# Optimization experiments

Measured on AMD Instinct MI355X. Metric: run time of the kernel, lower is better.

The kernel has to match this reference:

```python
import jax, jax.numpy as jnp
import numpy as np

N_NODES = 10000
IN_FEAT = 512
OUT_FEAT = 512
N_EDGES = 160000


def setup_inputs() -> dict:
    key = jax.random.key(0)
    kx, kw, ks, kd = jax.random.split(key, 4)
    x = jax.random.normal(kx, (N_NODES, IN_FEAT), dtype=jnp.float32)
    # Xavier-uniform init for w: shape [out_features, 2*in_features]
    fan_in, fan_out = 2 * IN_FEAT, OUT_FEAT
    limit = float(np.sqrt(6.0 / (fan_in + fan_out)))
    w = jax.random.uniform(kw, (OUT_FEAT, 2 * IN_FEAT), dtype=jnp.float32,
                           minval=-limit, maxval=limit)
    src = jax.random.randint(ks, (N_EDGES,), 0, N_NODES, dtype=jnp.int32)
    dst = jax.random.randint(kd, (N_EDGES,), 0, N_NODES, dtype=jnp.int32)
    edge_index = jnp.stack([src, dst], axis=0)  # [2, E]
    return {"x": x, "w": w, "edge_index": edge_index}


def reference(x, w, edge_index):
    # GraphSAGE-mean layer: h = relu(W @ concat(x, mean_{j in N(i)} x_j))
    src, dst = edge_index[0], edge_index[1]
    msgs = x[src]  # [E, F] gather of neighbor features
    summed = jax.ops.segment_sum(msgs, dst, num_segments=x.shape[0])  # [N, F]
    deg = jax.ops.segment_sum(jnp.ones_like(dst, dtype=x.dtype), dst,
                              num_segments=x.shape[0])  # [N]
    neighbor_mean = summed / jnp.maximum(deg, 1.0)[:, None]
    message = jnp.concatenate([x, neighbor_mean], axis=-1)  # [N, 2F]
    weighted = jnp.einsum('of,nf->no', w, message)  # [N, out]
    return jax.nn.relu(weighted)
```

## Files before the change

kernel.cpp:

```cpp
#include <hip/hip_runtime.h>
#include <hip/hip_bf16.h>

#define N_NODES 10000
#define IN_FEAT 512
#define OUT_FEAT 512
#define N_EDGES 160000
#define KDIM 1024
#define CAP 96

typedef __bf16 bf16x8 __attribute__((ext_vector_type(8)));
typedef float f32x4 __attribute__((ext_vector_type(4)));

#define AS1 __attribute__((address_space(1)))
#define AS3 __attribute__((address_space(3)))

__device__ __forceinline__ void async_copy16(void* lds, const void* g) {
    __builtin_amdgcn_global_load_lds((const AS1 unsigned int*)g,
                                     (AS3 unsigned int*)lds, 16, 0, 0);
}

__device__ __forceinline__ unsigned short f2bf(float f) {
    unsigned int u = __builtin_bit_cast(unsigned int, f);
    u += 0x7fffu + ((u >> 16) & 1u);
    return (unsigned short)(u >> 16);
}


__global__ __launch_bounds__(256) void k_zero(int* __restrict__ cnt) {
    int i = blockIdx.x * 256 + threadIdx.x;
    if (i < N_NODES / 4) ((int4*)cnt)[i] = (int4){0, 0, 0, 0};
}


#define PREP_EDGE_BLOCKS ((N_EDGES + 255) / 256)
#define PREP_W_BLOCKS (OUT_FEAT * KDIM / 8 / 256)
#define PREP_X_BLOCKS (N_NODES * IN_FEAT / 8 / 256)
#define PREP_BLOCKS (PREP_EDGE_BLOCKS + PREP_W_BLOCKS + PREP_X_BLOCKS)

__device__ __forceinline__ void cvt8(const float* __restrict__ src,
                                     unsigned short* __restrict__ dst, int i) {
    const float4* sp = (const float4*)(src + (size_t)i * 8);
    float4 a = sp[0], b = sp[1];
    uint4 o;
    o.x = (unsigned)f2bf(a.x) | ((unsigned)f2bf(a.y) << 16);
    o.y = (unsigned)f2bf(a.z) | ((unsigned)f2bf(a.w) << 16);
    o.z = (unsigned)f2bf(b.x) | ((unsigned)f2bf(b.y) << 16);
    o.w = (unsigned)f2bf(b.z) | ((unsigned)f2bf(b.w) << 16);
    *(uint4*)(dst + (size_t)i * 8) = o;
}

__global__ __launch_bounds__(256) void k_prep(
    const float* __restrict__ x, const float* __restrict__ w,
    const int* __restrict__ ei, int* __restrict__ cnt,
    int* __restrict__ bucket, unsigned short* __restrict__ xb,
    unsigned short* __restrict__ wb) {
    int b = blockIdx.x;
    if (b < PREP_EDGE_BLOCKS) {
        int e = b * 256 + threadIdx.x;
        if (e < N_EDGES) {
            int s = ei[e];
            int d = ei[N_EDGES + e];
            int slot = atomicAdd(&cnt[d], 1);
            if (slot < CAP) bucket[d * CAP + slot] = s;
        }
    } else if (b < PREP_EDGE_BLOCKS + PREP_W_BLOCKS) {
        int i = (b - PREP_EDGE_BLOCKS) * 256 + threadIdx.x;
        cvt8(w, wb, i);
    } else {
        int i = (b - PREP_EDGE_BLOCKS - PREP_W_BLOCKS) * 256 + threadIdx.x;
        cvt8(x, xb, i);
    }
}


__device__ __forceinline__ void accum8(float* acc, uint4 v) {
    unsigned d[4] = {v.x, v.y, v.z, v.w};
#pragma unroll
    for (int j = 0; j < 4; ++j) {
        acc[2 * j]     += __builtin_bit_cast(float, d[j] << 16);
        acc[2 * j + 1] += __builtin_bit_cast(float, d[j] & 0xffff0000u);
    }
}

__global__ __launch_bounds__(256) void k_aggregate(
    const unsigned short* __restrict__ xb, const int* __restrict__ cnt,
    const int* __restrict__ bucket, unsigned short* __restrict__ mb) {
    int wid = (blockIdx.x * 256 + threadIdx.x) >> 6;
    int lane = threadIdx.x & 63;
    if (wid >= N_NODES) return;
    int deg = cnt[wid];
    int n = deg < CAP ? deg : CAP;
    const int4* brow = (const int4*)(bucket + wid * CAP);
    const unsigned short* xrow = xb + lane * 8;
    float acc[8] = {0.f, 0.f, 0.f, 0.f, 0.f, 0.f, 0.f, 0.f};
    int e = 0;
    for (; e + 8 <= n; e += 8) {
        int4 i0 = brow[e >> 2];
        int4 i1 = brow[(e >> 2) + 1];
        uint4 v0 = *(const uint4*)(xrow + (size_t)i0.x * IN_FEAT);
        uint4 v1 = *(const uint4*)(xrow + (size_t)i0.y * IN_FEAT);
        uint4 v2 = *(const uint4*)(xrow + (size_t)i0.z * IN_FEAT);
        uint4 v3 = *(const uint4*)(xrow + (size_t)i0.w * IN_FEAT);
        uint4 v4 = *(const uint4*)(xrow + (size_t)i1.x * IN_FEAT);
        uint4 v5 = *(const uint4*)(xrow + (size_t)i1.y * IN_FEAT);
        uint4 v6 = *(const uint4*)(xrow + (size_t)i1.z * IN_FEAT);
        uint4 v7 = *(const uint4*)(xrow + (size_t)i1.w * IN_FEAT);
        accum8(acc, v0); accum8(acc, v1); accum8(acc, v2); accum8(acc, v3);
        accum8(acc, v4); accum8(acc, v5); accum8(acc, v6); accum8(acc, v7);
    }
    if (e + 4 <= n) {
        int4 i0 = brow[e >> 2];
        uint4 v0 = *(const uint4*)(xrow + (size_t)i0.x * IN_FEAT);
        uint4 v1 = *(const uint4*)(xrow + (size_t)i0.y * IN_FEAT);
        uint4 v2 = *(const uint4*)(xrow + (size_t)i0.z * IN_FEAT);
        uint4 v3 = *(const uint4*)(xrow + (size_t)i0.w * IN_FEAT);
        accum8(acc, v0); accum8(acc, v1); accum8(acc, v2); accum8(acc, v3);
        e += 4;
    }
    for (; e < n; ++e) {
        int s = bucket[wid * CAP + e];
        uint4 v = *(const uint4*)(xrow + (size_t)s * IN_FEAT);
        accum8(acc, v);
    }
    float inv = 1.0f / fmaxf((float)deg, 1.0f);
    uint4 o;
    o.x = (unsigned)f2bf(acc[0] * inv) | ((unsigned)f2bf(acc[1] * inv) << 16);
    o.y = (unsigned)f2bf(acc[2] * inv) | ((unsigned)f2bf(acc[3] * inv) << 16);
    o.z = (unsigned)f2bf(acc[4] * inv) | ((unsigned)f2bf(acc[5] * inv) << 16);
    o.w = (unsigned)f2bf(acc[6] * inv) | ((unsigned)f2bf(acc[7] * inv) << 16);
    *(uint4*)(mb + (size_t)wid * IN_FEAT + lane * 8) = o;
}


#define BM 64
#define BN 128
#define BK 64

__global__ __launch_bounds__(256) void k_gemm(const unsigned short* __restrict__ xb,
                                              const unsigned short* __restrict__ mb,
                                              const unsigned short* __restrict__ wb,
                                              float* __restrict__ out) {
    __shared__ unsigned short As[BM * BK];
    __shared__ unsigned short Bs[BN * BK];
    const int tid = threadIdx.x;
    const int lane = tid & 63;
    const int w = tid >> 6;
    const int m0 = blockIdx.x * BM;
    const int n0 = blockIdx.y * BN;

    const int wr = w >> 1, wc = w & 1;

    const int st_sub = lane >> 3;
    const int st_col = (lane & 7) * 8;

    f32x4 acc[2][4];
#pragma unroll
    for (int m = 0; m < 2; ++m)
#pragma unroll
        for (int n = 0; n < 4; ++n) acc[m][n] = (f32x4){0.f, 0.f, 0.f, 0.f};

    for (int k0 = 0; k0 < KDIM; k0 += BK) {
        const unsigned short* abase = (k0 < IN_FEAT) ? xb : mb;
        const int kc = (k0 < IN_FEAT) ? k0 : (k0 - IN_FEAT);
#pragma unroll
        for (int i = 0; i < 2; ++i) {
            int row = w * 16 + i * 8 + st_sub;
            int rg = m0 + row;
            if (rg > N_NODES - 1) rg = N_NODES - 1;
            async_copy16(&As[(w * 16 + i * 8) * BK],
                         abase + (size_t)rg * IN_FEAT + kc + st_col);
        }
#pragma unroll
        for (int i = 0; i < 4; ++i) {
            int row = w * 32 + i * 8 + st_sub;
            async_copy16(&Bs[(w * 32 + i * 8) * BK],
                         wb + (size_t)(n0 + row) * KDIM + k0 + st_col);
        }
        __syncthreads();

#pragma unroll
        for (int kk = 0; kk < 2; ++kk) {
            bf16x8 a[2], b[4];
            const int krow = kk * 32 + (lane >> 4) * 8;
#pragma unroll
            for (int m = 0; m < 2; ++m) {
                int r = wr * 32 + m * 16 + (lane & 15);
                a[m] = *(const bf16x8*)&As[r * BK + krow];
            }
#pragma unroll
            for (int n = 0; n < 4; ++n) {
                int r = wc * 64 + n * 16 + (lane & 15);
                b[n] = *(const bf16x8*)&Bs[r * BK + krow];
            }
#pragma unroll
            for (int m = 0; m < 2; ++m)
#pragma unroll
                for (int n = 0; n < 4; ++n)
                    acc[m][n] = __builtin_amdgcn_mfma_f32_16x16x32_bf16(
                        a[m], b[n], acc[m][n], 0, 0, 0);
        }
        __syncthreads();
    }

    const int col_in = lane & 15;
    const int rquad = (lane >> 4) * 4;
#pragma unroll
    for (int m = 0; m < 2; ++m) {
#pragma unroll
        for (int n = 0; n < 4; ++n) {
#pragma unroll
            for (int r = 0; r < 4; ++r) {
                int mg = m0 + wr * 32 + m * 16 + rquad + r;
                int og = n0 + wc * 64 + n * 16 + col_in;
                if (mg < N_NODES) {
                    float v = acc[m][n][r];
                    out[(size_t)mg * OUT_FEAT + og] = v > 0.f ? v : 0.f;
                }
            }
        }
    }
}


extern "C" void kernel_launch(void* const* d_in, const int* in_sizes, int n_in,
                              void* d_out, int out_size, void* d_ws, size_t ws_size,
                              hipStream_t stream) {
    const float* x = (const float*)d_in[0];
    const float* w = (const float*)d_in[1];
    const int* ei = (const int*)d_in[2];
    float* out = (float*)d_out;

    char* ws = (char*)d_ws;
    const size_t XB_OFF = 0;
    const size_t MB_OFF = XB_OFF + (size_t)N_NODES * IN_FEAT * 2;
    const size_t WB_OFF = MB_OFF + (size_t)N_NODES * IN_FEAT * 2;
    const size_t CNT_OFF = WB_OFF + (size_t)OUT_FEAT * KDIM * 2;
    const size_t BKT_OFF = CNT_OFF + (size_t)N_NODES * 4;

    unsigned short* xb = (unsigned short*)(ws + XB_OFF);
    unsigned short* mb = (unsigned short*)(ws + MB_OFF);
    unsigned short* wb = (unsigned short*)(ws + WB_OFF);
    int* cnt = (int*)(ws + CNT_OFF);
    int* bucket = (int*)(ws + BKT_OFF);

    k_zero<<<(N_NODES / 4 + 255) / 256, 256, 0, stream>>>(cnt);
    k_prep<<<PREP_BLOCKS, 256, 0, stream>>>(x, w, ei, cnt, bucket, xb, wb);
    k_aggregate<<<(N_NODES * 64 + 255) / 256, 256, 0, stream>>>(xb, cnt, bucket, mb);
    dim3 ggrid((N_NODES + BM - 1) / BM, OUT_FEAT / BN);
    k_gemm<<<ggrid, 256, 0, stream>>>(xb, mb, wb, out);
}
```

Measured before the change: 71.93 us.

## Split aggregation across feature chunks and swizzle GEMM tile order for locality

The aggregation kernel now spreads each node over four blocks along a second grid dimension. Each lane loads one 32-bit word (two bf16 values) per neighbor instead of a 16-byte vector, which raises the number of waves in flight and cuts per-thread register pressure. The GEMM launch becomes a 1D grid with a swizzled mapping that groups 8 M-tiles with all 4 N-tiles, so neighboring blocks share A and B tiles in cache; blocks past the last M-tile exit early. In exchange, each gather load is narrower, so more load instructions and more bucket index reads are issued per byte of neighbor data.

```diff
diff --git a/kernel.cpp b/kernel.cpp
--- a/kernel.cpp
+++ b/kernel.cpp
@@ -23,6 +23,13 @@
     unsigned int u = __builtin_bit_cast(unsigned int, f);
     u += 0x7fffu + ((u >> 16) & 1u);
     return (unsigned short)(u >> 16);
+}
+
+__device__ __forceinline__ float bflo(unsigned v) {
+    return __builtin_bit_cast(float, v << 16);
+}
+__device__ __forceinline__ float bfhi(unsigned v) {
+    return __builtin_bit_cast(float, v & 0xffff0000u);
 }
 
 
@@ -73,68 +80,59 @@
 }
 
 
-__device__ __forceinline__ void accum8(float* acc, uint4 v) {
-    unsigned d[4] = {v.x, v.y, v.z, v.w};
-#pragma unroll
-    for (int j = 0; j < 4; ++j) {
-        acc[2 * j]     += __builtin_bit_cast(float, d[j] << 16);
-        acc[2 * j + 1] += __builtin_bit_cast(float, d[j] & 0xffff0000u);
-    }
-}
-
 __global__ __launch_bounds__(256) void k_aggregate(
     const unsigned short* __restrict__ xb, const int* __restrict__ cnt,
     const int* __restrict__ bucket, unsigned short* __restrict__ mb) {
-    int wid = (blockIdx.x * 256 + threadIdx.x) >> 6;
-    int lane = threadIdx.x & 63;
-    if (wid >= N_NODES) return;
-    int deg = cnt[wid];
-    int n = deg < CAP ? deg : CAP;
-    const int4* brow = (const int4*)(bucket + wid * CAP);
-    const unsigned short* xrow = xb + lane * 8;
-    float acc[8] = {0.f, 0.f, 0.f, 0.f, 0.f, 0.f, 0.f, 0.f};
+    const int chunk = blockIdx.y;
+    const int node = blockIdx.x * 4 + (threadIdx.x >> 6);
+    const int lane = threadIdx.x & 63;
+    const int deg = cnt[node];
+    const int n = deg < CAP ? deg : CAP;
+    const int4* brow = (const int4*)(bucket + node * CAP);
+    const unsigned* xcol = (const unsigned*)xb + chunk * 64 + lane;
+    float a0 = 0.f, a1 = 0.f;
     int e = 0;
     for (; e + 8 <= n; e += 8) {
         int4 i0 = brow[e >> 2];
         int4 i1 = brow[(e >> 2) + 1];
-        uint4 v0 = *(const uint4*)(xrow + (size_t)i0.x * IN_FEAT);
-        uint4 v1 = *(const uint4*)(xrow + (size_t)i0.y * IN_FEAT);
-        uint4 v2 = *(const uint4*)(xrow + (size_t)i0.z * IN_FEAT);
-        uint4 v3 = *(const uint4*)(xrow + (size_t)i0.w * IN_FEAT);
-        uint4 v4 = *(const uint4*)(xrow + (size_t)i1.x * IN_FEAT);
-        uint4 v5 = *(const uint4*)(xrow + (size_t)i1.y * IN_FEAT);
-        uint4 v6 = *(const uint4*)(xrow + (size_t)i1.z * IN_FEAT);
-        uint4 v7 = *(const uint4*)(xrow + (size_t)i1.w * IN_FEAT);
-        accum8(acc, v0); accum8(acc, v1); accum8(acc, v2); accum8(acc, v3);
-        accum8(acc, v4); accum8(acc, v5); accum8(acc, v6); accum8(acc, v7);
+        unsigned v0 = xcol[(size_t)i0.x * 256];
+        unsigned v1 = xcol[(size_t)i0.y * 256];
+        unsigned v2 = xcol[(size_t)i0.z * 256];
+        unsigned v3 = xcol[(size_t)i0.w * 256];
+        unsigned v4 = xcol[(size_t)i1.x * 256];
+        unsigned v5 = xcol[(size_t)i1.y * 256];
+        unsigned v6 = xcol[(size_t)i1.z * 256];
+        unsigned v7 = xcol[(size_t)i1.w * 256];
+        a0 += bflo(v0) + bflo(v1) + bflo(v2) + bflo(v3) +
+              bflo(v4) + bflo(v5) + bflo(v6) + bflo(v7);
+        a1 += bfhi(v0) + bfhi(v1) + bfhi(v2) + bfhi(v3) +
+              bfhi(v4) + bfhi(v5) + bfhi(v6) + bfhi(v7);
     }
     if (e + 4 <= n) {
         int4 i0 = brow[e >> 2];
-        uint4 v0 = *(const uint4*)(xrow + (size_t)i0.x * IN_FEAT);
-        uint4 v1 = *(const uint4*)(xrow + (size_t)i0.y * IN_FEAT);
-        uint4 v2 = *(const uint4*)(xrow + (size_t)i0.z * IN_FEAT);
-        uint4 v3 = *(const uint4*)(xrow + (size_t)i0.w * IN_FEAT);
-        accum8(acc, v0); accum8(acc, v1); accum8(acc, v2); accum8(acc, v3);
+        unsigned v0 = xcol[(size_t)i0.x * 256];
+        unsigned v1 = xcol[(size_t)i0.y * 256];
+        unsigned v2 = xcol[(size_t)i0.z * 256];
+        unsigned v3 = xcol[(size_t)i0.w * 256];
+        a0 += bflo(v0) + bflo(v1) + bflo(v2) + bflo(v3);
+        a1 += bfhi(v0) + bfhi(v1) + bfhi(v2) + bfhi(v3);
         e += 4;
     }
     for (; e < n; ++e) {
-        int s = bucket[wid * CAP + e];
-        uint4 v = *(const uint4*)(xrow + (size_t)s * IN_FEAT);
-        accum8(acc, v);
+        unsigned v = xcol[(size_t)bucket[node * CAP + e] * 256];
+        a0 += bflo(v);
+        a1 += bfhi(v);
     }
     float inv = 1.0f / fmaxf((float)deg, 1.0f);
-    uint4 o;
-    o.x = (unsigned)f2bf(acc[0] * inv) | ((unsigned)f2bf(acc[1] * inv) << 16);
-    o.y = (unsigned)f2bf(acc[2] * inv) | ((unsigned)f2bf(acc[3] * inv) << 16);
-    o.z = (unsigned)f2bf(acc[4] * inv) | ((unsigned)f2bf(acc[5] * inv) << 16);
-    o.w = (unsigned)f2bf(acc[6] * inv) | ((unsigned)f2bf(acc[7] * inv) << 16);
-    *(uint4*)(mb + (size_t)wid * IN_FEAT + lane * 8) = o;
+    unsigned o = (unsigned)f2bf(a0 * inv) | ((unsigned)f2bf(a1 * inv) << 16);
+    ((unsigned*)mb)[(size_t)node * 256 + chunk * 64 + lane] = o;
 }
 
 
 #define BM 64
 #define BN 128
 #define BK 64
+#define MT_PAD 160
 
 __global__ __launch_bounds__(256) void k_gemm(const unsigned short* __restrict__ xb,
                                               const unsigned short* __restrict__ mb,
@@ -142,12 +140,16 @@
                                               float* __restrict__ out) {
     __shared__ unsigned short As[BM * BK];
     __shared__ unsigned short Bs[BN * BK];
+    const int idx = blockIdx.x;
+    const int mt = (idx & 7) + 8 * (idx >> 5);
+    const int nt = (idx >> 3) & 3;
+    if (mt >= (N_NODES + BM - 1) / BM) return;
+    const int m0 = mt * BM;
+    const int n0 = nt * BN;
+
     const int tid = threadIdx.x;
     const int lane = tid & 63;
     const int w = tid >> 6;
-    const int m0 = blockIdx.x * BM;
-    const int n0 = blockIdx.y * BN;
-
     const int wr = w >> 1, wc = w & 1;
 
     const int st_sub = lane >> 3;
@@ -245,7 +247,7 @@
 
     k_zero<<<(N_NODES / 4 + 255) / 256, 256, 0, stream>>>(cnt);
     k_prep<<<PREP_BLOCKS, 256, 0, stream>>>(x, w, ei, cnt, bucket, xb, wb);
-    k_aggregate<<<(N_NODES * 64 + 255) / 256, 256, 0, stream>>>(xb, cnt, bucket, mb);
-    dim3 ggrid((N_NODES + BM - 1) / BM, OUT_FEAT / BN);
-    k_gemm<<<ggrid, 256, 0, stream>>>(xb, mb, wb, out);
-}
+    dim3 agrid(N_NODES / 4, 4);
+    k_aggregate<<<agrid, 256, 0, stream>>>(xb, cnt, bucket, mb);
+    k_gemm<<<(MT_PAD / 8) * 32, 256, 0, stream>>>(xb, mb, wb, out);
+}
```

New measurement: 73.40 us. 2.0% more time.

## Split neighbor aggregation across feature chunks and edge slots with shuffle reduction

Applied to the files above, without the earlier changes.

The aggregate kernel now gives each wavefront one node and one 128-feature chunk, with four lane groups each handling a different edge slot. Partial sums are combined with cross-lane xor shuffles before writing. This launches four times as many wavefronts with shorter dependent gather chains, aiming to raise memory-level parallelism and occupancy. The cost is extra shuffle work, repeated bucket index loads across chunks, and fewer loads in flight per lane.

```diff
diff --git a/kernel.cpp b/kernel.cpp
--- a/kernel.cpp
+++ b/kernel.cpp
@@ -85,50 +85,52 @@
 __global__ __launch_bounds__(256) void k_aggregate(
     const unsigned short* __restrict__ xb, const int* __restrict__ cnt,
     const int* __restrict__ bucket, unsigned short* __restrict__ mb) {
-    int wid = (blockIdx.x * 256 + threadIdx.x) >> 6;
-    int lane = threadIdx.x & 63;
-    if (wid >= N_NODES) return;
-    int deg = cnt[wid];
-    int n = deg < CAP ? deg : CAP;
-    const int4* brow = (const int4*)(bucket + wid * CAP);
-    const unsigned short* xrow = xb + lane * 8;
+    const int chunk = blockIdx.y;
+    const int node = blockIdx.x * 4 + (threadIdx.x >> 6);
+    const int lane = threadIdx.x & 63;
+    const int slot = lane >> 4;
+    const int fg = lane & 15;
+    const int deg = cnt[node];
+    const int n = deg < CAP ? deg : CAP;
+    const int bbase = node * CAP;
+    const unsigned short* xcol = xb + chunk * 128 + fg * 8;
     float acc[8] = {0.f, 0.f, 0.f, 0.f, 0.f, 0.f, 0.f, 0.f};
     int e = 0;
     for (; e + 8 <= n; e += 8) {
-        int4 i0 = brow[e >> 2];
-        int4 i1 = brow[(e >> 2) + 1];
-        uint4 v0 = *(const uint4*)(xrow + (size_t)i0.x * IN_FEAT);
-        uint4 v1 = *(const uint4*)(xrow + (size_t)i0.y * IN_FEAT);
-        uint4 v2 = *(const uint4*)(xrow + (size_t)i0.z * IN_FEAT);
-        uint4 v3 = *(const uint4*)(xrow + (size_t)i0.w * IN_FEAT);
-        uint4 v4 = *(const uint4*)(xrow + (size_t)i1.x * IN_FEAT);
-        uint4 v5 = *(const uint4*)(xrow + (size_t)i1.y * IN_FEAT);
-        uint4 v6 = *(const uint4*)(xrow + (size_t)i1.z * IN_FEAT);
-        uint4 v7 = *(const uint4*)(xrow + (size_t)i1.w * IN_FEAT);
-        accum8(acc, v0); accum8(acc, v1); accum8(acc, v2); accum8(acc, v3);
-        accum8(acc, v4); accum8(acc, v5); accum8(acc, v6); accum8(acc, v7);
+        int s0 = bucket[bbase + e + slot];
+        int s1 = bucket[bbase + e + 4 + slot];
+        uint4 v0 = *(const uint4*)(xcol + (size_t)s0 * IN_FEAT);
+        uint4 v1 = *(const uint4*)(xcol + (size_t)s1 * IN_FEAT);
+        accum8(acc, v0);
+        accum8(acc, v1);
     }
     if (e + 4 <= n) {
-        int4 i0 = brow[e >> 2];
-        uint4 v0 = *(const uint4*)(xrow + (size_t)i0.x * IN_FEAT);
-        uint4 v1 = *(const uint4*)(xrow + (size_t)i0.y * IN_FEAT);
-        uint4 v2 = *(const uint4*)(xrow + (size_t)i0.z * IN_FEAT);
-        uint4 v3 = *(const uint4*)(xrow + (size_t)i0.w * IN_FEAT);
-        accum8(acc, v0); accum8(acc, v1); accum8(acc, v2); accum8(acc, v3);
+        int s0 = bucket[bbase + e + slot];
+        uint4 v0 = *(const uint4*)(xcol + (size_t)s0 * IN_FEAT);
+        accum8(acc, v0);
         e += 4;
     }
-    for (; e < n; ++e) {
-        int s = bucket[wid * CAP + e];
-        uint4 v = *(const uint4*)(xrow + (size_t)s * IN_FEAT);
-        accum8(acc, v);
-    }
-    float inv = 1.0f / fmaxf((float)deg, 1.0f);
-    uint4 o;
-    o.x = (unsigned)f2bf(acc[0] * inv) | ((unsigned)f2bf(acc[1] * inv) << 16);
-    o.y = (unsigned)f2bf(acc[2] * inv) | ((unsigned)f2bf(acc[3] * inv) << 16);
-    o.z = (unsigned)f2bf(acc[4] * inv) | ((unsigned)f2bf(acc[5] * inv) << 16);
-    o.w = (unsigned)f2bf(acc[6] * inv) | ((unsigned)f2bf(acc[7] * inv) << 16);
-    *(uint4*)(mb + (size_t)wid * IN_FEAT + lane * 8) = o;
+    int rem = n - e;
+    if (rem > 0) {
+        int ss = slot < rem ? slot : rem - 1;
+        int s0 = bucket[bbase + e + ss];
+        uint4 v0 = *(const uint4*)(xcol + (size_t)s0 * IN_FEAT);
+        if (slot < rem) accum8(acc, v0);
+    }
+#pragma unroll
+    for (int j = 0; j < 8; ++j) {
+        acc[j] += __shfl_xor(acc[j], 16, 64);
+        acc[j] += __shfl_xor(acc[j], 32, 64);
+    }
+    if (lane < 16) {
+        float inv = 1.0f / fmaxf((float)deg, 1.0f);
+        uint4 o;
+        o.x = (unsigned)f2bf(acc[0] * inv) | ((unsigned)f2bf(acc[1] * inv) << 16);
+        o.y = (unsigned)f2bf(acc[2] * inv) | ((unsigned)f2bf(acc[3] * inv) << 16);
+        o.z = (unsigned)f2bf(acc[4] * inv) | ((unsigned)f2bf(acc[5] * inv) << 16);
+        o.w = (unsigned)f2bf(acc[6] * inv) | ((unsigned)f2bf(acc[7] * inv) << 16);
+        *(uint4*)(mb + (size_t)node * IN_FEAT + chunk * 128 + fg * 8) = o;
+    }
 }
 
 
@@ -245,7 +247,8 @@
 
     k_zero<<<(N_NODES / 4 + 255) / 256, 256, 0, stream>>>(cnt);
     k_prep<<<PREP_BLOCKS, 256, 0, stream>>>(x, w, ei, cnt, bucket, xb, wb);
-    k_aggregate<<<(N_NODES * 64 + 255) / 256, 256, 0, stream>>>(xb, cnt, bucket, mb);
+    dim3 agrid(N_NODES / 4, 4);
+    k_aggregate<<<agrid, 256, 0, stream>>>(xb, cnt, bucket, mb);
     dim3 ggrid((N_NODES + BM - 1) / BM, OUT_FEAT / BN);
     k_gemm<<<ggrid, 256, 0, stream>>>(xb, mb, wb, out);
 }
```

Measured after the change: 73.39 us. 1.02x slower.
